# Optimization experiments

Hardware: AMD Instinct MI355X
Metric: run time of the kernel (lower is better)

Reference implementation:

```python
import jax, jax.numpy as jnp
import numpy as np

L = 4; B = 128; S = 128; N = B * S; E = 262144
IN = 64; HID = 128; PE = 16; HEADS = 4; DK = HID // HEADS; OUT = 10


def setup_inputs() -> dict:
    key = jax.random.key(0)
    ks = iter(jax.random.split(key, 64))
    def nrm(shape, scale=1.0):
        return jax.random.normal(next(ks), shape, jnp.float32) * scale
    inp = {
        'x': nrm((N, IN)),
        'pe': nrm((N, PE)),
        'edge_attr': nrm((E, HID)),
        'sph': jax.random.uniform(next(ks), (B, 1, S, S), jnp.float32),
        'node_w': nrm((IN, HID - PE), 0.05), 'node_b': jnp.zeros((HID - PE,), jnp.float32),
        'pe_w': nrm((PE, PE), 0.05), 'pe_b': jnp.zeros((PE,), jnp.float32),
        'conv_Aw': nrm((L, HID, HID), 0.05), 'conv_Ab': jnp.zeros((L, HID), jnp.float32),
        'conv_Bw': nrm((L, HID, HID), 0.05), 'conv_Bb': jnp.zeros((L, HID), jnp.float32),
        'conv_Cw': nrm((L, HID, HID), 0.05), 'conv_Cb': jnp.zeros((L, HID), jnp.float32),
        'conv_Dw': nrm((L, HID, HID), 0.05), 'conv_Db': jnp.zeros((L, HID), jnp.float32),
        'conv_Ew': nrm((L, HID, HID), 0.05), 'conv_Eb': jnp.zeros((L, HID), jnp.float32),
        'bnx_g': jnp.ones((L, HID), jnp.float32), 'bnx_b': jnp.zeros((L, HID), jnp.float32),
        'bne_g': jnp.ones((L, HID), jnp.float32), 'bne_b': jnp.zeros((L, HID), jnp.float32),
        'attn_w': nrm((4, HID, HID), 0.05), 'attn_b': jnp.zeros((4, HID), jnp.float32),
        'mlp1_w': nrm((HID, HID // 2), 0.05), 'mlp1_b': jnp.zeros((HID // 2,), jnp.float32),
        'mlp2_w': nrm((HID // 2, HID // 4), 0.05), 'mlp2_b': jnp.zeros((HID // 4,), jnp.float32),
        'mlp3_w': nrm((HID // 4, OUT), 0.05), 'mlp3_b': jnp.zeros((OUT,), jnp.float32),
        'edge_index': jax.random.randint(next(ks), (2, E), 0, N, dtype=jnp.int32),
        'batch': jnp.repeat(jnp.arange(B, dtype=jnp.int32), S),  # equal-size graphs, sorted
    }
    return inp


def _bn(v, g, b):
    # BatchNorm1d in training mode (batch statistics), eps=1e-5
    mu = v.mean(0)
    var = jnp.mean((v - mu) ** 2, 0)
    return g * (v - mu) * jax.lax.rsqrt(var + 1e-5) + b


def _forward(x, pe, edge_attr, sph, node_w, node_b, pe_w, pe_b,
             conv_Aw, conv_Ab, conv_Bw, conv_Bb, conv_Cw, conv_Cb,
             conv_Dw, conv_Db, conv_Ew, conv_Eb,
             bnx_g, bnx_b, bne_g, bne_b, attn_w, attn_b,
             mlp1_w, mlp1_b, mlp2_w, mlp2_b, mlp3_w, mlp3_b,
             edge_index, batch):
    src, dst = edge_index[0], edge_index[1]  # message j->i: index = dst
    h = jnp.concatenate([x @ node_w + node_b, pe @ pe_w + pe_b], axis=-1)  # [N, HID]
    e = edge_attr
    inv_sqrt_dk = np.float32(1.0 / np.sqrt(DK))
    for l in range(L):
        # ---- GatedGCNConv (residual, aggr='add' with sigmoid-gated normalization) ----
        Ax = h @ conv_Aw[l] + conv_Ab[l]
        Bx = h @ conv_Bw[l] + conv_Bb[l]
        Ce = e @ conv_Cw[l] + conv_Cb[l]
        Dx = h @ conv_Dw[l] + conv_Db[l]
        Ex = h @ conv_Ew[l] + conv_Eb[l]
        e_ij = Dx[dst] + Ex[src] + Ce               # [E, HID] pre-sigmoid edge feature
        sigma = jax.nn.sigmoid(e_ij)
        num = jax.ops.segment_sum(sigma * Bx[src], dst, num_segments=N)
        den = jax.ops.segment_sum(sigma, dst, num_segments=N)
        h_new = Ax + num / (den + 1e-6)
        h = jax.nn.relu(_bn(h_new, bnx_g[l], bnx_b[l])) + h
        e = jax.nn.relu(_bn(e_ij, bne_g[l], bne_b[l])) + e
        # ---- dense MHA with sph score bias (to_dense_batch == reshape, equal-size graphs) ----
        xd = h.reshape(B, S, HID)
        q = (xd @ attn_w[0] + attn_b[0]).reshape(B, S, HEADS, DK).transpose(0, 2, 1, 3)
        k = (xd @ attn_w[1] + attn_b[1]).reshape(B, S, HEADS, DK).transpose(0, 2, 1, 3)
        v = (xd @ attn_w[2] + attn_b[2]).reshape(B, S, HEADS, DK).transpose(0, 2, 1, 3)
        scores = jnp.einsum('bhsd,bhtd->bhst', q, k) * inv_sqrt_dk
        p = jax.nn.softmax(scores * sph, axis=-1)
        o = jnp.einsum('bhst,bhtd->bhsd', p, v).transpose(0, 2, 1, 3).reshape(B, S, HID)
        h = (o @ attn_w[3] + attn_b[3]).reshape(N, HID)
    # global mean pool over each graph
    g = jax.ops.segment_sum(h, batch, num_segments=B) / np.float32(S)
    g = jax.nn.relu(g @ mlp1_w + mlp1_b)
    g = jax.nn.relu(g @ mlp2_w + mlp2_b)
    return g @ mlp3_w + mlp3_b  # [B, OUT]


def reference(x, pe, edge_attr, sph, node_w, node_b, pe_w, pe_b,
              conv_Aw, conv_Ab, conv_Bw, conv_Bb, conv_Cw, conv_Cb,
              conv_Dw, conv_Db, conv_Ew, conv_Eb,
              bnx_g, bnx_b, bne_g, bne_b, attn_w, attn_b,
              mlp1_w, mlp1_b, mlp2_w, mlp2_b, mlp3_w, mlp3_b,
              edge_index, batch):
    return _forward(x, pe, edge_attr, sph, node_w, node_b, pe_w, pe_b,
                    conv_Aw, conv_Ab, conv_Bw, conv_Bb, conv_Cw, conv_Cb,
                    conv_Dw, conv_Db, conv_Ew, conv_Eb,
                    bnx_g, bnx_b, bne_g, bne_b, attn_w, attn_b,
                    mlp1_w, mlp1_b, mlp2_w, mlp2_b, mlp3_w, mlp3_b,
                    edge_index, batch)
```

## Files before the change

### kernel.cpp

```cpp
#include <hip/hip_runtime.h>
#include <math.h>

#define L_LAYERS 4
#define B_G 128
#define S_G 128
#define N_N 16384
#define E_E 262144
#define IN_F 64
#define HID 128
#define PE_F 16
#define HEADS 4
#define DK 32
#define OUT_F 10

typedef __bf16 bf16x8 __attribute__((ext_vector_type(8)));
typedef float f32x4 __attribute__((ext_vector_type(4)));

struct Sel4 { float* o[4]; const float* b[4]; int slot[4]; };
struct WSrc24 { const float* w[24]; };

__global__ void zero_int_kernel(int* __restrict__ p, int n) {
    int i = blockIdx.x * 256 + threadIdx.x;
    if (i < n) p[i] = 0;
}

__global__ void hist_kernel(const int* __restrict__ dst, int* __restrict__ deg) {
    int e = blockIdx.x * 256 + threadIdx.x;
    if (e < E_E) atomicAdd(&deg[dst[e]], 1);
}

__global__ __launch_bounds__(1024) void scan_kernel(const int* __restrict__ deg,
                                                    int* __restrict__ row_ptr,
                                                    int* __restrict__ cursor) {
    __shared__ int lds[1024];
    int tid = threadIdx.x;
    int base = tid * 16;
    int d[16];
    int s = 0;
#pragma unroll
    for (int i = 0; i < 16; i++) { d[i] = deg[base + i]; s += d[i]; }
    lds[tid] = s;
    __syncthreads();
    for (int off = 1; off < 1024; off <<= 1) {
        int v = (tid >= off) ? lds[tid - off] : 0;
        __syncthreads();
        lds[tid] += v;
        __syncthreads();
    }
    int run = lds[tid] - s;
#pragma unroll
    for (int i = 0; i < 16; i++) {
        row_ptr[base + i] = run;
        cursor[base + i] = run;
        run += d[i];
    }
    if (tid == 1023) row_ptr[N_N] = run;
}

__global__ void scatter_kernel(const int* __restrict__ src, const int* __restrict__ dst,
                               int* __restrict__ cursor, int* __restrict__ perm,
                               int* __restrict__ ssrc, int* __restrict__ sdst) {
    int e = blockIdx.x * 256 + threadIdx.x;
    if (e >= E_E) return;
    int dd = dst[e];
    int pos = atomicAdd(&cursor[dd], 1);
    perm[pos] = e;
    ssrc[pos] = src[e];
    sdst[pos] = dd;
}

__global__ __launch_bounds__(256) void pack_w_kernel(WSrc24 ws, __bf16* __restrict__ Whi,
                                                     __bf16* __restrict__ Wlo) {
    int m = blockIdx.x;
    const float* W = ws.w[m];
    int tid = threadIdx.x;
    for (int i = 0; i < 64; i++) {
        int p = i * 256 + tid;
        int j = p & 7, lane = (p >> 3) & 63, kc = (p >> 9) & 3, nt = p >> 11;
        int k = kc * 32 + (lane >> 4) * 8 + j;
        int n = nt * 16 + (lane & 15);
        float w = W[k * 128 + n];
        __bf16 h = (__bf16)w;
        Whi[(long)m * 16384 + p] = h;
        Wlo[(long)m * 16384 + p] = (__bf16)(w - (float)h);
    }
}

__global__ void embed_kernel(const float* __restrict__ x, const float* __restrict__ pe,
                             const float* __restrict__ node_w, const float* __restrict__ node_b,
                             const float* __restrict__ pe_w, const float* __restrict__ pe_b,
                             float* __restrict__ h) {
    int idx = blockIdx.x * 256 + threadIdx.x;
    if (idx >= N_N * HID) return;
    int i = idx >> 7, c = idx & 127;
    float acc;
    if (c < 112) {
        acc = node_b[c];
        const float* xr = x + (long)i * IN_F;
        for (int k = 0; k < IN_F; k++) acc += xr[k] * node_w[k * 112 + c];
    } else {
        int cc = c - 112;
        acc = pe_b[cc];
        const float* pr = pe + (long)i * PE_F;
        for (int k = 0; k < PE_F; k++) acc += pr[k] * pe_w[k * PE_F + cc];
    }
    h[idx] = acc;
}

template <int MODE>
__global__ __launch_bounds__(256) void mfma_gemm_ws_kernel(
    const float* __restrict__ A, const int* __restrict__ perm,
    const __bf16* __restrict__ Whi, const __bf16* __restrict__ Wlo, Sel4 sel,
    const float* __restrict__ Dx, const float* __restrict__ Ex,
    const int* __restrict__ sdst, const int* __restrict__ ssrc,
    float* __restrict__ stats_acc, int ntiles) {
    __shared__ float sred[256];
    int tid = threadIdx.x;
    int lane = tid & 63, wave = tid >> 6;
    int l15 = lane & 15, quad = lane >> 4;
    int y = blockIdx.y;
    float* out = sel.o[y];
    const float* bias = sel.b[y];
    const bf16x8* whv = (const bf16x8*)(Whi + (long)sel.slot[y] * 16384);
    const bf16x8* wlv = (const bf16x8*)(Wlo + (long)sel.slot[y] * 16384);

    bf16x8 bh[2][4], bl[2][4];
#pragma unroll
    for (int ntl = 0; ntl < 2; ntl++)
#pragma unroll
        for (int kc = 0; kc < 4; kc++) {
            int fi = ((2 * wave + ntl) * 4 + kc) * 64 + lane;
            bh[ntl][kc] = whv[fi];
            bl[ntl][kc] = wlv[fi];
        }

    int c0 = (2 * wave) * 16 + l15, c1 = (2 * wave + 1) * 16 + l15;
    float bias0 = bias[c0], bias1 = bias[c1];

    float csum[2] = {0.f, 0.f}, csq[2] = {0.f, 0.f};

    for (int t = blockIdx.x; t < ntiles; t += gridDim.x) {
        long rowA = (long)t * 16 + l15;
        if (MODE == 1 && perm) rowA = perm[rowA];
        const float* Ap = A + rowA * 128 + quad * 8;

        f32x4 acc0 = (f32x4){0.f, 0.f, 0.f, 0.f};
        f32x4 acc1 = (f32x4){0.f, 0.f, 0.f, 0.f};
#pragma unroll
        for (int kc = 0; kc < 4; kc++) {
            float4 a0 = *(const float4*)(Ap + kc * 32);
            float4 a1 = *(const float4*)(Ap + kc * 32 + 4);
            float fv[8] = {a0.x, a0.y, a0.z, a0.w, a1.x, a1.y, a1.z, a1.w};
            bf16x8 ahi, alo;
#pragma unroll
            for (int j = 0; j < 8; j++) {
                __bf16 hh = (__bf16)fv[j];
                ahi[j] = hh;
                alo[j] = (__bf16)(fv[j] - (float)hh);
            }
            acc0 = __builtin_amdgcn_mfma_f32_16x16x32_bf16(ahi, bl[0][kc], acc0, 0, 0, 0);
            acc1 = __builtin_amdgcn_mfma_f32_16x16x32_bf16(ahi, bl[1][kc], acc1, 0, 0, 0);
            acc0 = __builtin_amdgcn_mfma_f32_16x16x32_bf16(alo, bh[0][kc], acc0, 0, 0, 0);
            acc1 = __builtin_amdgcn_mfma_f32_16x16x32_bf16(alo, bh[1][kc], acc1, 0, 0, 0);
            acc0 = __builtin_amdgcn_mfma_f32_16x16x32_bf16(ahi, bh[0][kc], acc0, 0, 0, 0);
            acc1 = __builtin_amdgcn_mfma_f32_16x16x32_bf16(ahi, bh[1][kc], acc1, 0, 0, 0);
        }

        long rb = (long)t * 16 + quad * 4;
        if (MODE == 1) {
            int sd[4], ss[4];
#pragma unroll
            for (int r = 0; r < 4; r++) { sd[r] = sdst[rb + r]; ss[r] = ssrc[rb + r]; }
#pragma unroll
            for (int r = 0; r < 4; r++) {
                float v0 = acc0[r] + bias0 + Dx[(long)sd[r] * 128 + c0] + Ex[(long)ss[r] * 128 + c0];
                float v1 = acc1[r] + bias1 + Dx[(long)sd[r] * 128 + c1] + Ex[(long)ss[r] * 128 + c1];
                out[(rb + r) * 128 + c0] = v0;
                out[(rb + r) * 128 + c1] = v1;
                csum[0] += v0; csq[0] += v0 * v0;
                csum[1] += v1; csq[1] += v1 * v1;
            }
        } else {
#pragma unroll
            for (int r = 0; r < 4; r++) {
                out[(rb + r) * 128 + c0] = acc0[r] + bias0;
                out[(rb + r) * 128 + c1] = acc1[r] + bias1;
            }
        }
    }

    if (MODE == 1) {
#pragma unroll
        for (int ntl = 0; ntl < 2; ntl++) {
            float s = csum[ntl];
            s += __shfl_xor(s, 16); s += __shfl_xor(s, 32);
            float q = csq[ntl];
            q += __shfl_xor(q, 16); q += __shfl_xor(q, 32);
            if (quad == 0) {
                int c = (2 * wave + ntl) * 16 + l15;
                sred[c] = s;
                sred[128 + c] = q;
            }
        }
        __syncthreads();
        atomicAdd(&stats_acc[tid], sred[tid]);
    }
}

__global__ void ebn_finalize_kernel(const float* __restrict__ acc, float invM,
                                    float* __restrict__ stat) {
    int c = threadIdx.x;
    float mu = acc[c] * invM;
    float var = acc[128 + c] * invM - mu * mu;
    stat[c] = mu;
    stat[128 + c] = rsqrtf(var + 1e-5f);
}

__global__ __launch_bounds__(256) void bn_stats_kernel(const float* __restrict__ v, long M,
                                                       float* __restrict__ partial) {
    __shared__ float lds[256];
    int tid = threadIdx.x;
    int c = tid & 127, half = tid >> 7;
    float sum = 0.f, sq = 0.f;
    for (long r = (long)blockIdx.x * 2 + half; r < M; r += (long)gridDim.x * 2) {
        float x = v[r * 128 + c];
        sum += x; sq += x * x;
    }
    lds[tid] = sum;
    __syncthreads();
    if (half == 0) sum += lds[tid + 128];
    __syncthreads();
    lds[tid] = sq;
    __syncthreads();
    if (half == 0) {
        sq += lds[tid + 128];
        partial[(long)blockIdx.x * 256 + c] = sum;
        partial[(long)blockIdx.x * 256 + 128 + c] = sq;
    }
}

__global__ void bn_finalize_kernel(const float* __restrict__ partial, int nblk, float invM,
                                   float* __restrict__ stat) {
    int c = threadIdx.x;
    float s = 0.f, q = 0.f;
    for (int i = 0; i < nblk; i++) {
        s += partial[i * 256 + c];
        q += partial[i * 256 + 128 + c];
    }
    float mu = s * invM;
    float var = q * invM - mu * mu;
    stat[c] = mu;
    stat[128 + c] = rsqrtf(var + 1e-5f);
}

__global__ void bn_apply_res_kernel(const float* __restrict__ vin, const float* __restrict__ stat,
                                    const float* __restrict__ g, const float* __restrict__ b,
                                    float* __restrict__ io, long M4) {
    long idx = (long)blockIdx.x * 256 + threadIdx.x;
    if (idx >= M4) return;
    int c4 = (idx & 31) << 2;
    float4 x = ((const float4*)vin)[idx];
    float4 res = ((float4*)io)[idx];
    float xv[4] = {x.x, x.y, x.z, x.w};
    float rv[4] = {res.x, res.y, res.z, res.w};
    float o[4];
#pragma unroll
    for (int t = 0; t < 4; t++) {
        int c = c4 + t;
        float y = g[c] * (xv[t] - stat[c]) * stat[128 + c] + b[c];
        o[t] = fmaxf(y, 0.f) + rv[t];
    }
    ((float4*)io)[idx] = make_float4(o[0], o[1], o[2], o[3]);
}

__global__ __launch_bounds__(256) void agg_bn_kernel(
    const float* __restrict__ eij, const float* __restrict__ Bx, const float* __restrict__ Ax,
    const int* __restrict__ row_ptr, const int* __restrict__ ssrc,
    const float* __restrict__ estat, const float* __restrict__ g, const float* __restrict__ b,
    const float* __restrict__ eold, const int* __restrict__ perm,
    float* __restrict__ e_out, float* __restrict__ hnew) {
    int wave = threadIdx.x >> 6, lane = threadIdx.x & 63;
    int i = blockIdx.x * 4 + wave;
    int c = lane << 1;
    int s0 = row_ptr[i], s1 = row_ptr[i + 1];
    float2 mu = *(const float2*)&estat[c];
    float2 rs = *(const float2*)&estat[128 + c];
    float2 gg = *(const float2*)&g[c];
    float2 bb = *(const float2*)&b[c];
    float nx = 0.f, ny = 0.f, dx = 0.f, dy = 0.f;

    int j = s0;
    for (; j + 2 <= s1; j += 2) {
        int src0 = ssrc[j], src1 = ssrc[j + 1];
        long er0 = perm ? (long)perm[j] : (long)j;
        long er1 = perm ? (long)perm[j + 1] : (long)(j + 1);
        float2 x0 = *(const float2*)&eij[(long)j * 128 + c];
        float2 x1 = *(const float2*)&eij[(long)(j + 1) * 128 + c];
        float2 bx0 = *(const float2*)&Bx[(long)src0 * 128 + c];
        float2 bx1 = *(const float2*)&Bx[(long)src1 * 128 + c];
        float2 o0 = *(const float2*)&eold[er0 * 128 + c];
        float2 o1 = *(const float2*)&eold[er1 * 128 + c];
        float s0x = 1.f / (1.f + __expf(-x0.x)), s0y = 1.f / (1.f + __expf(-x0.y));
        float s1x = 1.f / (1.f + __expf(-x1.x)), s1y = 1.f / (1.f + __expf(-x1.y));
        nx += s0x * bx0.x + s1x * bx1.x;
        ny += s0y * bx0.y + s1y * bx1.y;
        dx += s0x + s1x;
        dy += s0y + s1y;
        float2 y0, y1;
        y0.x = fmaxf(gg.x * (x0.x - mu.x) * rs.x + bb.x, 0.f) + o0.x;
        y0.y = fmaxf(gg.y * (x0.y - mu.y) * rs.y + bb.y, 0.f) + o0.y;
        y1.x = fmaxf(gg.x * (x1.x - mu.x) * rs.x + bb.x, 0.f) + o1.x;
        y1.y = fmaxf(gg.y * (x1.y - mu.y) * rs.y + bb.y, 0.f) + o1.y;
        *(float2*)&e_out[(long)j * 128 + c] = y0;
        *(float2*)&e_out[(long)(j + 1) * 128 + c] = y1;
    }
    if (j < s1) {
        int src0 = ssrc[j];
        long er0 = perm ? (long)perm[j] : (long)j;
        float2 x0 = *(const float2*)&eij[(long)j * 128 + c];
        float2 bx0 = *(const float2*)&Bx[(long)src0 * 128 + c];
        float2 o0 = *(const float2*)&eold[er0 * 128 + c];
        float s0x = 1.f / (1.f + __expf(-x0.x)), s0y = 1.f / (1.f + __expf(-x0.y));
        nx += s0x * bx0.x; ny += s0y * bx0.y;
        dx += s0x; dy += s0y;
        float2 y0;
        y0.x = fmaxf(gg.x * (x0.x - mu.x) * rs.x + bb.x, 0.f) + o0.x;
        y0.y = fmaxf(gg.y * (x0.y - mu.y) * rs.y + bb.y, 0.f) + o0.y;
        *(float2*)&e_out[(long)j * 128 + c] = y0;
    }

    long idx = (long)i * 128 + c;
    float2 ax = *(const float2*)&Ax[idx];
    float2 hv;
    hv.x = ax.x + nx / (dx + 1e-6f);
    hv.y = ax.y + ny / (dy + 1e-6f);
    *(float2*)&hnew[idx] = hv;
}

__global__ __launch_bounds__(256) void attn_kernel(const float* __restrict__ q,
                                                   const float* __restrict__ k,
                                                   const float* __restrict__ v,
                                                   const float* __restrict__ sph,
                                                   float* __restrict__ o) {
    __shared__ float k_lds[128 * 32];
    __shared__ float v_lds[128 * 32];
    int b = blockIdx.x >> 2, hd = blockIdx.x & 3;
    int tid = threadIdx.x;

    for (int i = tid; i < 1024; i += 256) {
        int t = i >> 3, d4 = i & 7;
        long gidx = (long)(b * 128 + t) * 32 + hd * 8 + d4;
        ((float4*)k_lds)[t * 8 + d4] = ((const float4*)k)[gidx];
        ((float4*)v_lds)[t * 8 + d4] = ((const float4*)v)[gidx];
    }
    __syncthreads();

    int s = tid >> 1, t0 = (tid & 1) * 64;
    float4 qreg[8];
    long qbase = (long)(b * 128 + s) * 32 + hd * 8;
#pragma unroll
    for (int j = 0; j < 8; j++) qreg[j] = ((const float4*)q)[qbase + j];
    const float* sphrow = sph + ((long)b * 128 + s) * 128 + t0;
    const float inv_sqrt_dk = 0.17677669529663687f;

    float p[64];
#pragma unroll
    for (int i = 0; i < 64; i++) {
        const float4* kr = (const float4*)&k_lds[(t0 + i) * 32];
        float acc = 0.f;
#pragma unroll
        for (int j = 0; j < 8; j++) {
            float4 kv = kr[j];
            acc += qreg[j].x * kv.x + qreg[j].y * kv.y + qreg[j].z * kv.z + qreg[j].w * kv.w;
        }
        p[i] = acc * inv_sqrt_dk * sphrow[i];
    }
    float m = -1e30f;
#pragma unroll
    for (int i = 0; i < 64; i++) m = fmaxf(m, p[i]);
    m = fmaxf(m, __shfl_xor(m, 1));
    float l = 0.f;
#pragma unroll
    for (int i = 0; i < 64; i++) {
        p[i] = __expf(p[i] - m);
        l += p[i];
    }
    l += __shfl_xor(l, 1);
    float invl = 1.f / l;

    float part[32];
#pragma unroll
    for (int d = 0; d < 32; d++) part[d] = 0.f;
#pragma unroll
    for (int i = 0; i < 64; i++) {
        float pv = p[i] * invl;
        const float4* vr = (const float4*)&v_lds[(t0 + i) * 32];
#pragma unroll
        for (int j = 0; j < 8; j++) {
            float4 vv = vr[j];
            part[4 * j + 0] += pv * vv.x;
            part[4 * j + 1] += pv * vv.y;
            part[4 * j + 2] += pv * vv.z;
            part[4 * j + 3] += pv * vv.w;
        }
    }
    int halfw = tid & 1;
    float outv[16];
#pragma unroll
    for (int d = 0; d < 32; d++) {
        float tot = part[d] + __shfl_xor(part[d], 1);
        if ((d >> 4) == halfw) outv[d & 15] = tot;
    }
    long obase = (long)(b * 128 + s) * 32 + hd * 8 + halfw * 4;
#pragma unroll
    for (int j = 0; j < 4; j++)
        ((float4*)o)[obase + j] = make_float4(outv[4 * j], outv[4 * j + 1], outv[4 * j + 2], outv[4 * j + 3]);
}

__global__ __launch_bounds__(128) void pool_mlp_kernel(
    const float* __restrict__ h, const float* __restrict__ w1, const float* __restrict__ b1,
    const float* __restrict__ w2, const float* __restrict__ b2, const float* __restrict__ w3,
    const float* __restrict__ b3, float* __restrict__ out) {
    __shared__ float g[128], m1[64], m2[32];
    int b = blockIdx.x, tid = threadIdx.x;
    const float* hb = h + (long)b * 128 * 128;
    float s = 0.f;
    for (int r = 0; r < 128; r++) s += hb[r * 128 + tid];
    g[tid] = s * (1.f / 128.f);
    __syncthreads();
    if (tid < 64) {
        float a = b1[tid];
        for (int kk = 0; kk < 128; kk++) a += g[kk] * w1[kk * 64 + tid];
        m1[tid] = fmaxf(a, 0.f);
    }
    __syncthreads();
    if (tid < 32) {
        float a = b2[tid];
        for (int kk = 0; kk < 64; kk++) a += m1[kk] * w2[kk * 32 + tid];
        m2[tid] = fmaxf(a, 0.f);
    }
    __syncthreads();
    if (tid < 10) {
        float a = b3[tid];
        for (int kk = 0; kk < 32; kk++) a += m2[kk] * w3[kk * 10 + tid];
        out[b * 10 + tid] = a;
    }
}

extern "C" void kernel_launch(void* const* d_in, const int* in_sizes, int n_in,
                              void* d_out, int out_size, void* d_ws, size_t ws_size,
                              hipStream_t stream) {
    (void)in_sizes; (void)n_in; (void)out_size;
    const float* x        = (const float*)d_in[0];
    const float* pe       = (const float*)d_in[1];
    const float* edge_attr= (const float*)d_in[2];
    const float* sph      = (const float*)d_in[3];
    const float* node_w   = (const float*)d_in[4];
    const float* node_b   = (const float*)d_in[5];
    const float* pe_w     = (const float*)d_in[6];
    const float* pe_b     = (const float*)d_in[7];
    const float* conv_Aw  = (const float*)d_in[8];
    const float* conv_Ab  = (const float*)d_in[9];
    const float* conv_Bw  = (const float*)d_in[10];
    const float* conv_Bb  = (const float*)d_in[11];
    const float* conv_Cw  = (const float*)d_in[12];
    const float* conv_Cb  = (const float*)d_in[13];
    const float* conv_Dw  = (const float*)d_in[14];
    const float* conv_Db  = (const float*)d_in[15];
    const float* conv_Ew  = (const float*)d_in[16];
    const float* conv_Eb  = (const float*)d_in[17];
    const float* bnx_g    = (const float*)d_in[18];
    const float* bnx_b    = (const float*)d_in[19];
    const float* bne_g    = (const float*)d_in[20];
    const float* bne_b    = (const float*)d_in[21];
    const float* attn_w   = (const float*)d_in[22];
    const float* attn_b   = (const float*)d_in[23];
    const float* mlp1_w   = (const float*)d_in[24];
    const float* mlp1_b   = (const float*)d_in[25];
    const float* mlp2_w   = (const float*)d_in[26];
    const float* mlp2_b   = (const float*)d_in[27];
    const float* mlp3_w   = (const float*)d_in[28];
    const float* mlp3_b   = (const float*)d_in[29];
    const int*   eidx     = (const int*)d_in[30];
    const int* esrc = eidx;
    const int* edst = eidx + E_E;
    float* out = (float*)d_out;

    float* f = (float*)d_ws;
    float* h      = f; f += (long)N_N * HID;
    float* hnew   = f; f += (long)N_N * HID;
    float* Ax     = f; f += (long)N_N * HID;
    float* Bx     = f; f += (long)N_N * HID;
    float* Dx     = f; f += (long)N_N * HID;
    float* Ex     = f; f += (long)N_N * HID;
    float* e      = f; f += (long)E_E * HID;
    float* eij    = f; f += (long)E_E * HID;
    float* partial= f; f += 512 * 256;
    float* bnxs   = f; f += 256;
    float* bnes   = f; f += 256;
    float* ebn_acc= f; f += 256;
    __bf16* Whi = (__bf16*)f;
    __bf16* Wlo = Whi + 24 * 16384;
    int* ip = (int*)(Wlo + 24 * 16384);
    int* deg     = ip; ip += N_N;
    int* row_ptr = ip; ip += N_N + 1;
    int* cursor  = ip; ip += N_N;
    int* perm    = ip; ip += E_E;
    int* ssrc    = ip; ip += E_E;
    int* sdst    = ip; ip += E_E;
    size_t need = (size_t)((char*)ip - (char*)d_ws);
    if (ws_size < need) return;

    WSrc24 wsrc;
    for (int l = 0; l < L_LAYERS; l++) {
        wsrc.w[l * 5 + 0] = conv_Aw + l * 16384;
        wsrc.w[l * 5 + 1] = conv_Bw + l * 16384;
        wsrc.w[l * 5 + 2] = conv_Cw + l * 16384;
        wsrc.w[l * 5 + 3] = conv_Dw + l * 16384;
        wsrc.w[l * 5 + 4] = conv_Ew + l * 16384;
    }
    for (int m = 0; m < 4; m++) wsrc.w[20 + m] = attn_w + m * 16384;
    pack_w_kernel<<<24, 256, 0, stream>>>(wsrc, Whi, Wlo);

    zero_int_kernel<<<(N_N + 255) / 256, 256, 0, stream>>>(deg, N_N);
    hist_kernel<<<E_E / 256, 256, 0, stream>>>(edst, deg);
    scan_kernel<<<1, 1024, 0, stream>>>(deg, row_ptr, cursor);
    scatter_kernel<<<E_E / 256, 256, 0, stream>>>(esrc, edst, cursor, perm, ssrc, sdst);

    embed_kernel<<<N_N * HID / 256, 256, 0, stream>>>(x, pe, node_w, node_b, pe_w, pe_b, h);

    for (int l = 0; l < L_LAYERS; l++) {
        zero_int_kernel<<<1, 256, 0, stream>>>((int*)ebn_acc, 256);

        Sel4 selN;
        selN.o[0] = Ax; selN.b[0] = conv_Ab + l * 128; selN.slot[0] = l * 5 + 0;
        selN.o[1] = Bx; selN.b[1] = conv_Bb + l * 128; selN.slot[1] = l * 5 + 1;
        selN.o[2] = Dx; selN.b[2] = conv_Db + l * 128; selN.slot[2] = l * 5 + 3;
        selN.o[3] = Ex; selN.b[3] = conv_Eb + l * 128; selN.slot[3] = l * 5 + 4;
        mfma_gemm_ws_kernel<0><<<dim3(512, 4), 256, 0, stream>>>(
            h, nullptr, Whi, Wlo, selN, nullptr, nullptr, nullptr, nullptr, nullptr, N_N / 16);

        const float* Asrc = (l == 0) ? edge_attr : e;
        const int* permA = (l == 0) ? perm : nullptr;
        Sel4 selE;
        selE.o[0] = eij; selE.b[0] = conv_Cb + l * 128; selE.slot[0] = l * 5 + 2;
        selE.o[1] = selE.o[2] = selE.o[3] = eij;
        selE.b[1] = selE.b[2] = selE.b[3] = selE.b[0];
        selE.slot[1] = selE.slot[2] = selE.slot[3] = selE.slot[0];
        mfma_gemm_ws_kernel<1><<<dim3(2048, 1), 256, 0, stream>>>(
            Asrc, permA, Whi, Wlo, selE, Dx, Ex, sdst, ssrc, ebn_acc, E_E / 16);

        ebn_finalize_kernel<<<1, 128, 0, stream>>>(ebn_acc, 1.f / E_E, bnes);

        const float* eoldSrc = (l == 0) ? edge_attr : e;
        const int* permE = (l == 0) ? perm : nullptr;
        agg_bn_kernel<<<N_N / 4, 256, 0, stream>>>(eij, Bx, Ax, row_ptr, ssrc, bnes,
                                                   bne_g + l * 128, bne_b + l * 128,
                                                   eoldSrc, permE, e, hnew);

        bn_stats_kernel<<<128, 256, 0, stream>>>(hnew, (long)N_N, partial);
        bn_finalize_kernel<<<1, 128, 0, stream>>>(partial, 128, 1.f / N_N, bnxs);
        bn_apply_res_kernel<<<N_N * 32 / 256, 256, 0, stream>>>(
            hnew, bnxs, bnx_g + l * 128, bnx_b + l * 128, h, (long)N_N * 32);

        Sel4 selQ;
        selQ.o[0] = Ax; selQ.b[0] = attn_b;       selQ.slot[0] = 20;
        selQ.o[1] = Bx; selQ.b[1] = attn_b + 128; selQ.slot[1] = 21;
        selQ.o[2] = Dx; selQ.b[2] = attn_b + 256; selQ.slot[2] = 22;
        selQ.o[3] = Dx; selQ.b[3] = attn_b + 256; selQ.slot[3] = 22;
        mfma_gemm_ws_kernel<0><<<dim3(683, 3), 256, 0, stream>>>(
            h, nullptr, Whi, Wlo, selQ, nullptr, nullptr, nullptr, nullptr, nullptr, N_N / 16);

        attn_kernel<<<B_G * HEADS, 256, 0, stream>>>(Ax, Bx, Dx, sph, Ex);

        Sel4 selP;
        selP.o[0] = h; selP.b[0] = attn_b + 384; selP.slot[0] = 23;
        selP.o[1] = selP.o[2] = selP.o[3] = h;
        selP.b[1] = selP.b[2] = selP.b[3] = selP.b[0];
        selP.slot[1] = selP.slot[2] = selP.slot[3] = selP.slot[0];
        mfma_gemm_ws_kernel<0><<<dim3(1024, 1), 256, 0, stream>>>(
            Ex, nullptr, Whi, Wlo, selP, nullptr, nullptr, nullptr, nullptr, nullptr, N_N / 16);
    }

    pool_mlp_kernel<<<B_G, 128, 0, stream>>>(h, mlp1_w, mlp1_b, mlp2_w, mlp2_b, mlp3_w, mlp3_b, out);
}
```

Before: 1.890 ms.

## Retile MFMA GEMM so each wave computes 32 rows by all columns

The split-bf16 MFMA GEMM no longer keeps two column tiles of weights in registers per wave with a grid-stride loop over 16-row tiles. Each block now owns 128 rows, and each wave loads and converts 32 rows of A once, then streams all eight weight column tiles from global/L2. This removes the four-fold redundant A loads and hi/lo conversion across waves, which matters most for the large gathered edge GEMM. The cost is more accumulator registers, repeated weight reads per wave, and fewer blocks for the node GEMMs. The weight-packing kernel is also split across four times as many blocks.

```diff
diff --git a/kernel.cpp b/kernel.cpp
--- a/kernel.cpp
+++ b/kernel.cpp
@@ -71,10 +71,10 @@
 
 __global__ __launch_bounds__(256) void pack_w_kernel(WSrc24 ws, __bf16* __restrict__ Whi,
                                                      __bf16* __restrict__ Wlo) {
-    int m = blockIdx.x;
+    int m = blockIdx.x >> 2, part = blockIdx.x & 3;
     const float* W = ws.w[m];
     int tid = threadIdx.x;
-    for (int i = 0; i < 64; i++) {
+    for (int i = part * 16; i < part * 16 + 16; i++) {
         int p = i * 256 + tid;
         int j = p & 7, lane = (p >> 3) & 63, kc = (p >> 9) & 3, nt = p >> 11;
         int k = kc * 32 + (lane >> 4) * 8 + j;
@@ -108,13 +108,13 @@
 }
 
 template <int MODE>
-__global__ __launch_bounds__(256) void mfma_gemm_ws_kernel(
+__global__ __launch_bounds__(256) void mfma_gemm_kernel(
     const float* __restrict__ A, const int* __restrict__ perm,
     const __bf16* __restrict__ Whi, const __bf16* __restrict__ Wlo, Sel4 sel,
     const float* __restrict__ Dx, const float* __restrict__ Ex,
     const int* __restrict__ sdst, const int* __restrict__ ssrc,
-    float* __restrict__ stats_acc, int ntiles) {
-    __shared__ float sred[256];
+    float* __restrict__ stats_acc) {
+    __shared__ float sred[1024];
     int tid = threadIdx.x;
     int lane = tid & 63, wave = tid >> 6;
     int l15 = lane & 15, quad = lane >> 4;
@@ -124,86 +124,102 @@
     const bf16x8* whv = (const bf16x8*)(Whi + (long)sel.slot[y] * 16384);
     const bf16x8* wlv = (const bf16x8*)(Wlo + (long)sel.slot[y] * 16384);
 
-    bf16x8 bh[2][4], bl[2][4];
-#pragma unroll
-    for (int ntl = 0; ntl < 2; ntl++)
+    long r0 = (long)blockIdx.x * 128 + wave * 32;
+    long ra0 = r0 + l15, ra1 = r0 + 16 + l15;
+    if (MODE == 1 && perm) { ra0 = perm[ra0]; ra1 = perm[ra1]; }
+
+    float4 av[2][8];
+    {
+        const float* Ap0 = A + ra0 * 128 + quad * 8;
+        const float* Ap1 = A + ra1 * 128 + quad * 8;
 #pragma unroll
         for (int kc = 0; kc < 4; kc++) {
-            int fi = ((2 * wave + ntl) * 4 + kc) * 64 + lane;
-            bh[ntl][kc] = whv[fi];
-            bl[ntl][kc] = wlv[fi];
-        }
-
-    int c0 = (2 * wave) * 16 + l15, c1 = (2 * wave + 1) * 16 + l15;
-    float bias0 = bias[c0], bias1 = bias[c1];
-
-    float csum[2] = {0.f, 0.f}, csq[2] = {0.f, 0.f};
-
-    for (int t = blockIdx.x; t < ntiles; t += gridDim.x) {
-        long rowA = (long)t * 16 + l15;
-        if (MODE == 1 && perm) rowA = perm[rowA];
-        const float* Ap = A + rowA * 128 + quad * 8;
-
-        f32x4 acc0 = (f32x4){0.f, 0.f, 0.f, 0.f};
-        f32x4 acc1 = (f32x4){0.f, 0.f, 0.f, 0.f};
+            av[0][kc * 2] = *(const float4*)(Ap0 + kc * 32);
+            av[0][kc * 2 + 1] = *(const float4*)(Ap0 + kc * 32 + 4);
+            av[1][kc * 2] = *(const float4*)(Ap1 + kc * 32);
+            av[1][kc * 2 + 1] = *(const float4*)(Ap1 + kc * 32 + 4);
+        }
+    }
+    bf16x8 ahi[2][4], alo[2][4];
+#pragma unroll
+    for (int t = 0; t < 2; t++)
 #pragma unroll
         for (int kc = 0; kc < 4; kc++) {
-            float4 a0 = *(const float4*)(Ap + kc * 32);
-            float4 a1 = *(const float4*)(Ap + kc * 32 + 4);
-            float fv[8] = {a0.x, a0.y, a0.z, a0.w, a1.x, a1.y, a1.z, a1.w};
-            bf16x8 ahi, alo;
+            float fv[8] = {av[t][kc * 2].x, av[t][kc * 2].y, av[t][kc * 2].z, av[t][kc * 2].w,
+                           av[t][kc * 2 + 1].x, av[t][kc * 2 + 1].y, av[t][kc * 2 + 1].z,
+                           av[t][kc * 2 + 1].w};
 #pragma unroll
             for (int j = 0; j < 8; j++) {
                 __bf16 hh = (__bf16)fv[j];
-                ahi[j] = hh;
-                alo[j] = (__bf16)(fv[j] - (float)hh);
+                ahi[t][kc][j] = hh;
+                alo[t][kc][j] = (__bf16)(fv[j] - (float)hh);
             }
-            acc0 = __builtin_amdgcn_mfma_f32_16x16x32_bf16(ahi, bl[0][kc], acc0, 0, 0, 0);
-            acc1 = __builtin_amdgcn_mfma_f32_16x16x32_bf16(ahi, bl[1][kc], acc1, 0, 0, 0);
-            acc0 = __builtin_amdgcn_mfma_f32_16x16x32_bf16(alo, bh[0][kc], acc0, 0, 0, 0);
-            acc1 = __builtin_amdgcn_mfma_f32_16x16x32_bf16(alo, bh[1][kc], acc1, 0, 0, 0);
-            acc0 = __builtin_amdgcn_mfma_f32_16x16x32_bf16(ahi, bh[0][kc], acc0, 0, 0, 0);
-            acc1 = __builtin_amdgcn_mfma_f32_16x16x32_bf16(ahi, bh[1][kc], acc1, 0, 0, 0);
-        }
-
-        long rb = (long)t * 16 + quad * 4;
+        }
+
+    f32x4 acc[2][8];
+#pragma unroll
+    for (int t = 0; t < 2; t++)
+#pragma unroll
+        for (int nt = 0; nt < 8; nt++) acc[t][nt] = (f32x4){0.f, 0.f, 0.f, 0.f};
+
+#pragma unroll
+    for (int nt = 0; nt < 8; nt++) {
+#pragma unroll
+        for (int kc = 0; kc < 4; kc++) {
+            bf16x8 bhi = whv[(nt * 4 + kc) * 64 + lane];
+            bf16x8 blo = wlv[(nt * 4 + kc) * 64 + lane];
+            acc[0][nt] = __builtin_amdgcn_mfma_f32_16x16x32_bf16(ahi[0][kc], blo, acc[0][nt], 0, 0, 0);
+            acc[1][nt] = __builtin_amdgcn_mfma_f32_16x16x32_bf16(ahi[1][kc], blo, acc[1][nt], 0, 0, 0);
+            acc[0][nt] = __builtin_amdgcn_mfma_f32_16x16x32_bf16(alo[0][kc], bhi, acc[0][nt], 0, 0, 0);
+            acc[1][nt] = __builtin_amdgcn_mfma_f32_16x16x32_bf16(alo[1][kc], bhi, acc[1][nt], 0, 0, 0);
+            acc[0][nt] = __builtin_amdgcn_mfma_f32_16x16x32_bf16(ahi[0][kc], bhi, acc[0][nt], 0, 0, 0);
+            acc[1][nt] = __builtin_amdgcn_mfma_f32_16x16x32_bf16(ahi[1][kc], bhi, acc[1][nt], 0, 0, 0);
+        }
+    }
+
+    float csum[8], csq[8];
+#pragma unroll
+    for (int nt = 0; nt < 8; nt++) { csum[nt] = 0.f; csq[nt] = 0.f; }
+
+#pragma unroll
+    for (int t = 0; t < 2; t++) {
+        long rb = r0 + t * 16 + quad * 4;
+        int sd[4], ss[4];
         if (MODE == 1) {
-            int sd[4], ss[4];
 #pragma unroll
             for (int r = 0; r < 4; r++) { sd[r] = sdst[rb + r]; ss[r] = ssrc[rb + r]; }
+        }
+#pragma unroll
+        for (int nt = 0; nt < 8; nt++) {
+            int c = nt * 16 + l15;
+            float bb = bias[c];
 #pragma unroll
             for (int r = 0; r < 4; r++) {
-                float v0 = acc0[r] + bias0 + Dx[(long)sd[r] * 128 + c0] + Ex[(long)ss[r] * 128 + c0];
-                float v1 = acc1[r] + bias1 + Dx[(long)sd[r] * 128 + c1] + Ex[(long)ss[r] * 128 + c1];
-                out[(rb + r) * 128 + c0] = v0;
-                out[(rb + r) * 128 + c1] = v1;
-                csum[0] += v0; csq[0] += v0 * v0;
-                csum[1] += v1; csq[1] += v1 * v1;
+                float v = acc[t][nt][r] + bb;
+                if (MODE == 1) v += Dx[(long)sd[r] * 128 + c] + Ex[(long)ss[r] * 128 + c];
+                out[(rb + r) * 128 + c] = v;
+                if (MODE == 1) { csum[nt] += v; csq[nt] += v * v; }
             }
-        } else {
-#pragma unroll
-            for (int r = 0; r < 4; r++) {
-                out[(rb + r) * 128 + c0] = acc0[r] + bias0;
-                out[(rb + r) * 128 + c1] = acc1[r] + bias1;
-            }
         }
     }
 
     if (MODE == 1) {
 #pragma unroll
-        for (int ntl = 0; ntl < 2; ntl++) {
-            float s = csum[ntl];
+        for (int nt = 0; nt < 8; nt++) {
+            float s = csum[nt];
             s += __shfl_xor(s, 16); s += __shfl_xor(s, 32);
-            float q = csq[ntl];
+            float q = csq[nt];
             q += __shfl_xor(q, 16); q += __shfl_xor(q, 32);
             if (quad == 0) {
-                int c = (2 * wave + ntl) * 16 + l15;
-                sred[c] = s;
-                sred[128 + c] = q;
+                sred[wave * 256 + nt * 16 + l15] = s;
+                sred[wave * 256 + 128 + nt * 16 + l15] = q;
             }
         }
         __syncthreads();
-        atomicAdd(&stats_acc[tid], sred[tid]);
+        if (tid < 256) {
+            float v = sred[tid] + sred[256 + tid] + sred[512 + tid] + sred[768 + tid];
+            atomicAdd(&stats_acc[tid], v);
+        }
     }
 }
 
@@ -520,7 +536,7 @@
         wsrc.w[l * 5 + 4] = conv_Ew + l * 16384;
     }
     for (int m = 0; m < 4; m++) wsrc.w[20 + m] = attn_w + m * 16384;
-    pack_w_kernel<<<24, 256, 0, stream>>>(wsrc, Whi, Wlo);
+    pack_w_kernel<<<96, 256, 0, stream>>>(wsrc, Whi, Wlo);
 
     zero_int_kernel<<<(N_N + 255) / 256, 256, 0, stream>>>(deg, N_N);
     hist_kernel<<<E_E / 256, 256, 0, stream>>>(edst, deg);
@@ -537,8 +553,8 @@
         selN.o[1] = Bx; selN.b[1] = conv_Bb + l * 128; selN.slot[1] = l * 5 + 1;
         selN.o[2] = Dx; selN.b[2] = conv_Db + l * 128; selN.slot[2] = l * 5 + 3;
         selN.o[3] = Ex; selN.b[3] = conv_Eb + l * 128; selN.slot[3] = l * 5 + 4;
-        mfma_gemm_ws_kernel<0><<<dim3(512, 4), 256, 0, stream>>>(
-            h, nullptr, Whi, Wlo, selN, nullptr, nullptr, nullptr, nullptr, nullptr, N_N / 16);
+        mfma_gemm_kernel<0><<<dim3(N_N / 128, 4), 256, 0, stream>>>(
+            h, nullptr, Whi, Wlo, selN, nullptr, nullptr, nullptr, nullptr, nullptr);
 
         const float* Asrc = (l == 0) ? edge_attr : e;
         const int* permA = (l == 0) ? perm : nullptr;
@@ -547,8 +563,8 @@
         selE.o[1] = selE.o[2] = selE.o[3] = eij;
         selE.b[1] = selE.b[2] = selE.b[3] = selE.b[0];
         selE.slot[1] = selE.slot[2] = selE.slot[3] = selE.slot[0];
-        mfma_gemm_ws_kernel<1><<<dim3(2048, 1), 256, 0, stream>>>(
-            Asrc, permA, Whi, Wlo, selE, Dx, Ex, sdst, ssrc, ebn_acc, E_E / 16);
+        mfma_gemm_kernel<1><<<dim3(E_E / 128, 1), 256, 0, stream>>>(
+            Asrc, permA, Whi, Wlo, selE, Dx, Ex, sdst, ssrc, ebn_acc);
 
         ebn_finalize_kernel<<<1, 128, 0, stream>>>(ebn_acc, 1.f / E_E, bnes);
 
@@ -568,8 +584,8 @@
         selQ.o[1] = Bx; selQ.b[1] = attn_b + 128; selQ.slot[1] = 21;
         selQ.o[2] = Dx; selQ.b[2] = attn_b + 256; selQ.slot[2] = 22;
         selQ.o[3] = Dx; selQ.b[3] = attn_b + 256; selQ.slot[3] = 22;
-        mfma_gemm_ws_kernel<0><<<dim3(683, 3), 256, 0, stream>>>(
-            h, nullptr, Whi, Wlo, selQ, nullptr, nullptr, nullptr, nullptr, nullptr, N_N / 16);
+        mfma_gemm_kernel<0><<<dim3(N_N / 128, 3), 256, 0, stream>>>(
+            h, nullptr, Whi, Wlo, selQ, nullptr, nullptr, nullptr, nullptr, nullptr);
 
         attn_kernel<<<B_G * HEADS, 256, 0, stream>>>(Ax, Bx, Dx, sph, Ex);
 
@@ -578,8 +594,8 @@
         selP.o[1] = selP.o[2] = selP.o[3] = h;
         selP.b[1] = selP.b[2] = selP.b[3] = selP.b[0];
         selP.slot[1] = selP.slot[2] = selP.slot[3] = selP.slot[0];
-        mfma_gemm_ws_kernel<0><<<dim3(1024, 1), 256, 0, stream>>>(
-            Ex, nullptr, Whi, Wlo, selP, nullptr, nullptr, nullptr, nullptr, nullptr, N_N / 16);
+        mfma_gemm_kernel<0><<<dim3(N_N / 128, 1), 256, 0, stream>>>(
+            Ex, nullptr, Whi, Wlo, selP, nullptr, nullptr, nullptr, nullptr, nullptr);
     }
 
     pool_mlp_kernel<<<B_G, 128, 0, stream>>>(h, mlp1_w, mlp1_b, mlp2_w, mlp2_b, mlp3_w, mlp3_b, out);
```

Measured after the change: 2.050 ms. +8.4%, slower.
